# Performance work log

Hardware: AMD Instinct MI355X
Metric: run time of the kernel (lower is better)

## Reference

```python
import jax, jax.numpy as jnp
import numpy as np

# Config
D = 2048; H = 16; HD = 128; L = 2; V = 32000
BS = 16              # KV-cache block (page) size
B = 16               # decode batch (one query token per sequence)
MAXCTX = 1024; NBLK = MAXCTX // BS; NUMBLOCKS = B * NBLK
FF = 4 * D           # swiglu ff_proj width; ff_out input = FF // 2
ALIBI_BIAS_MAX = 8.0
EPS = 1e-5
NEG = -1e30


def alibi_slopes(n_heads, bias_max):
    # n_heads=16 is a power of two -> simple form
    m = jnp.arange(1, n_heads + 1, dtype=jnp.float32) * (bias_max / n_heads)
    return 1.0 / jnp.power(2.0, m)


def ln(x):
    # non-parametric LayerNorm (OLMo default: no affine, no bias)
    mu = jnp.mean(x, axis=-1, keepdims=True)
    var = jnp.var(x, axis=-1, keepdims=True)
    return (x - mu) * jax.lax.rsqrt(var + EPS)


def setup_inputs() -> dict:
    key = jax.random.key(0)
    ks = jax.random.split(key, 12)
    # context_lens includes the current (query) token; >= 1
    context_lens = jax.random.randint(ks[0], (B,), 1, MAXCTX + 1).astype(jnp.int32)
    positions = context_lens - 1                      # 0-indexed position of query token
    block_tables = jnp.arange(B * NBLK, dtype=jnp.int32).reshape(B, NBLK)
    slot_mapping = (block_tables[jnp.arange(B), positions // BS] * BS
                    + positions % BS).astype(jnp.int32)
    input_ids = jax.random.randint(ks[1], (B,), 0, V).astype(jnp.int32)
    s = 0.02
    return {
        "input_ids": input_ids,
        "positions": positions,
        "block_tables": block_tables,
        "context_lens": context_lens,
        "slot_mapping": slot_mapping,
        "wte": jax.random.normal(ks[2], (V, D), jnp.float32) * s,
        "Wq": jax.random.normal(ks[3], (L, D, D), jnp.float32) * s,
        "Wkv": jax.random.normal(ks[4], (L, D, 2 * HD), jnp.float32) * s,
        "Wo": jax.random.normal(ks[5], (L, D, D), jnp.float32) * s,
        "Wff1": jax.random.normal(ks[6], (L, D, FF), jnp.float32) * s,
        "Wff2": jax.random.normal(ks[7], (L, FF // 2, D), jnp.float32) * s,
        "k_caches": jax.random.normal(ks[8], (L, NUMBLOCKS, BS, H, HD), jnp.float32) * 0.1,
        "v_caches": jax.random.normal(ks[9], (L, NUMBLOCKS, BS, H, HD), jnp.float32) * 0.1,
    }


def reference(input_ids, positions, block_tables, context_lens, slot_mapping,
              wte, Wq, Wkv, Wo, Wff1, Wff2, k_caches, v_caches):
    scale = HD ** -0.5
    slopes = alibi_slopes(H, ALIBI_BIAS_MAX)          # [H]
    blk = slot_mapping // BS
    off = slot_mapping % BS
    pos = jnp.arange(MAXCTX)                          # [S]
    valid = pos[None, :] < context_lens[:, None]      # [B,S]
    # ALiBi decode bias: slope * (pos - (ctx_len-1)) for pos < ctx_len
    bias = slopes[None, :, None] * (pos[None, None, :]
            - (context_lens - 1)[:, None, None]).astype(jnp.float32)  # [B,H,S]

    x = wte[input_ids]                                # [B,D]
    for l in range(L):
        t = ln(x)
        q = (t @ Wq[l]).reshape(B, H, HD)
        kv = t @ Wkv[l]
        k_new, v_new = kv[:, :HD], kv[:, HD:]
        # MQA: single kv head repeated across H heads (as k.repeat(1, n_heads))
        k_rep = jnp.broadcast_to(k_new[:, None, :], (B, H, HD))
        v_rep = jnp.broadcast_to(v_new[:, None, :], (B, H, HD))
        # write current token's k/v into paged cache
        kc = k_caches[l].at[blk, off].set(k_rep)      # [NUMBLOCKS,BS,H,HD]
        vc = v_caches[l].at[blk, off].set(v_rep)
        # gather pages per sequence -> [B, MAXCTX, H, HD]
        keys = kc[block_tables].reshape(B, MAXCTX, H, HD)
        vals = vc[block_tables].reshape(B, MAXCTX, H, HD)
        scores = jnp.einsum('bhd,bshd->bhs', q, keys) * scale + bias
        scores = jnp.where(valid[:, None, :], scores, NEG)
        attn = jax.nn.softmax(scores, axis=-1)
        out = jnp.einsum('bhs,bshd->bhd', attn, vals).reshape(B, D)
        x = x + out @ Wo[l]
        h = ln(x) @ Wff1[l]                           # [B,FF]
        a, g = jnp.split(h, 2, axis=-1)               # swiglu: silu(gate) * x
        x = x + (jax.nn.silu(g) * a) @ Wff2[l]
    x = ln(x)
    return x @ wte.T                                  # tied-embedding logits [B,V]
```

## Files before the change

### kernel.cpp

```cpp
#include <hip/hip_runtime.h>
#include <hip/hip_bf16.h>
#include <math.h>

#define D 2048
#define H_ 16
#define HD 128
#define L_ 2
#define V_ 32000
#define BS_ 16
#define B_ 16
#define MAXCTX 1024
#define NBLK 64
#define FF 8192
#define SPLITS 8
#define CHUNK 128

__global__ void ln_kernel(const float* __restrict__ X,
                          const int* __restrict__ ids,
                          const float* __restrict__ wte,
                          float* __restrict__ Xout,
                          float* __restrict__ T,
                          float* __restrict__ Z, int zfloats) {
  if (blockIdx.x >= B_) {
    int nb = gridDim.x - B_;
    int idx = (blockIdx.x - B_) * 256 + threadIdx.x;
    int n4 = zfloats >> 2;
    float4* z4 = (float4*)Z;
    for (int i = idx; i < n4; i += nb * 256) z4[i] = make_float4(0.f, 0.f, 0.f, 0.f);
    return;
  }
  __shared__ float red[8];
  int b = blockIdx.x, tid = threadIdx.x;
  int wid = tid >> 6, lane = tid & 63;
  const float4* src = (const float4*)(ids ? (wte + (size_t)ids[b] * D) : (X + (size_t)b * D));
  float4 v0 = src[tid], v1 = src[tid + 256];
  if (ids) {
    float4* xo = (float4*)(Xout + (size_t)b * D);
    xo[tid] = v0; xo[tid + 256] = v1;
  }
  float s = v0.x + v0.y + v0.z + v0.w + v1.x + v1.y + v1.z + v1.w;
#pragma unroll
  for (int m = 32; m; m >>= 1) s += __shfl_xor(s, m);
  if (lane == 0) red[wid] = s;
  __syncthreads();
  float mu = (red[0] + red[1] + red[2] + red[3]) * (1.f / D);
  float d0 = v0.x - mu, d1 = v0.y - mu, d2 = v0.z - mu, d3 = v0.w - mu;
  float d4 = v1.x - mu, d5 = v1.y - mu, d6 = v1.z - mu, d7 = v1.w - mu;
  float vs = d0*d0 + d1*d1 + d2*d2 + d3*d3 + d4*d4 + d5*d5 + d6*d6 + d7*d7;
#pragma unroll
  for (int m = 32; m; m >>= 1) vs += __shfl_xor(vs, m);
  if (lane == 0) red[4 + wid] = vs;
  __syncthreads();
  float var = (red[4] + red[5] + red[6] + red[7]) * (1.f / D);
  float r = 1.f / sqrtf(var + 1e-5f);
  float4* t4 = (float4*)(T + (size_t)b * D);
  t4[tid]       = make_float4(d0 * r, d1 * r, d2 * r, d3 * r);
  t4[tid + 256] = make_float4(d4 * r, d5 * r, d6 * r, d7 * r);
}

#define GEMM_CORE_STORE(TL, WP, NSTRIDE, OPTR, J)                                  \
  {                                                                                \
    float acc[16];                                                                 \
    _Pragma("unroll") for (int b = 0; b < 16; b++) acc[b] = 0.f;                   \
    const float* wp_ = (WP);                                                       \
    _Pragma("unroll 4") for (int k = 0; k < 64; k++) {                             \
      float w = wp_[(size_t)k * (NSTRIDE)];                                        \
      const float4* tr = (const float4*)(&TL[k][0]);                               \
      float4 t0 = tr[0], t1 = tr[1], t2 = tr[2], t3 = tr[3];                       \
      acc[0]  += t0.x * w; acc[1]  += t0.y * w; acc[2]  += t0.z * w; acc[3]  += t0.w * w; \
      acc[4]  += t1.x * w; acc[5]  += t1.y * w; acc[6]  += t1.z * w; acc[7]  += t1.w * w; \
      acc[8]  += t2.x * w; acc[9]  += t2.y * w; acc[10] += t2.z * w; acc[11] += t2.w * w; \
      acc[12] += t3.x * w; acc[13] += t3.y * w; acc[14] += t3.z * w; acc[15] += t3.w * w; \
    }                                                                              \
    _Pragma("unroll") for (int b = 0; b < 16; b++)                                 \
      atomicAdd(&(OPTR)[(size_t)b * (NSTRIDE) + (J)], acc[b]);                     \
  }

__global__ void gemm_acc_kernel(const float* __restrict__ T,
                                const float* __restrict__ W,
                                float* __restrict__ O,
                                int K, int N) {
  __shared__ __align__(16) float tl[64][20];
  int tid = threadIdx.x;
  int j = blockIdx.x * 256 + tid;
  int k0 = blockIdx.y * 64;
#pragma unroll
  for (int r = 0; r < 4; r++) {
    int ii = tid + r * 256;
    int b = ii >> 6, k = ii & 63;
    tl[k][b] = T[(size_t)b * K + k0 + k];
  }
  __syncthreads();
  GEMM_CORE_STORE(tl, W + (size_t)k0 * N + j, N, O, j)
}

__global__ void qkv_gemm_kernel(const float* __restrict__ T,
                                const float* __restrict__ Wq,
                                const float* __restrict__ Wkv,
                                float* __restrict__ Qo,
                                float* __restrict__ KVo) {
  __shared__ __align__(16) float tl[64][20];
  int tid = threadIdx.x;
  int k0 = blockIdx.y * 64;
#pragma unroll
  for (int r = 0; r < 4; r++) {
    int ii = tid + r * 256;
    int b = ii >> 6, k = ii & 63;
    tl[k][b] = T[(size_t)b * D + k0 + k];
  }
  __syncthreads();
  if (blockIdx.x < 8) {
    int j = blockIdx.x * 256 + tid;
    GEMM_CORE_STORE(tl, Wq + (size_t)k0 * D + j, D, Qo, j)
  } else {
    int j = tid;
    GEMM_CORE_STORE(tl, Wkv + (size_t)k0 * 256 + j, 256, KVo, j)
  }
}

__global__ void attn_split_kernel(const float* __restrict__ Q,
                                  const float* __restrict__ KVn,
                                  const float* __restrict__ KC,
                                  const float* __restrict__ VC,
                                  const int* __restrict__ BT,
                                  const int* __restrict__ CL,
                                  float* __restrict__ Pout,
                                  float* __restrict__ Pms) {
  int bh = blockIdx.x, sp = blockIdx.y;
  int b = bh >> 4, h = bh & 15;
  int ctx = CL[b];
  int s0 = sp * CHUNK;
  if (s0 >= ctx) return;
  int s1 = min(s0 + CHUNK, ctx);
  int n = s1 - s0;
  int last = ctx - 1;
  int tid = threadIdx.x, wid = tid >> 6, lane = tid & 63;
  int half = lane >> 5, l32 = lane & 31;
  __shared__ float sc[CHUNK];
  __shared__ int btl[8];
  __shared__ float4 red[4][64];
  __shared__ float stat[8];
  if (tid < 8) btl[tid] = BT[b * NBLK + sp * 8 + tid];
  __syncthreads();
  float slope = exp2f(-0.5f * (float)(h + 1));
  const float scl = 0.08838834764831845f;
  float4 q4 = ((const float4*)(Q + (size_t)b * D + h * HD))[l32];

  for (int base = s0 + wid * 2; base < s1; base += 8) {
    int ps = base + half;
    if (ps < s1) {
      const float* kp = (ps == last) ? KVn + b * 256
                      : KC + ((size_t)btl[(ps - s0) >> 4] * BS_ + (ps & 15)) * (H_ * HD) + h * HD;
      float4 k4 = ((const float4*)kp)[l32];
      float p = q4.x * k4.x + q4.y * k4.y + q4.z * k4.z + q4.w * k4.w;
#pragma unroll
      for (int m = 16; m; m >>= 1) p += __shfl_xor(p, m);
      if (l32 == 0) sc[ps - s0] = p * scl + slope * (float)(ps - last);
    }
  }
  __syncthreads();

  float mx = -1e30f;
  for (int i = tid; i < n; i += 256) mx = fmaxf(mx, sc[i]);
#pragma unroll
  for (int m = 32; m; m >>= 1) mx = fmaxf(mx, __shfl_xor(mx, m));
  if (lane == 0) stat[wid] = mx;
  __syncthreads();
  mx = fmaxf(fmaxf(stat[0], stat[1]), fmaxf(stat[2], stat[3]));
  float sum = 0.f;
  for (int i = tid; i < n; i += 256) { float e = expf(sc[i] - mx); sc[i] = e; sum += e; }
#pragma unroll
  for (int m = 32; m; m >>= 1) sum += __shfl_xor(sum, m);
  if (lane == 0) stat[4 + wid] = sum;
  __syncthreads();

  float4 a4 = make_float4(0.f, 0.f, 0.f, 0.f);
  for (int base = s0 + wid * 2; base < s1; base += 8) {
    int ps = base + half;
    if (ps < s1) {
      const float* vp = (ps == last) ? KVn + b * 256 + HD
                      : VC + ((size_t)btl[(ps - s0) >> 4] * BS_ + (ps & 15)) * (H_ * HD) + h * HD;
      float4 v4 = ((const float4*)vp)[l32];
      float p = sc[ps - s0];
      a4.x += p * v4.x; a4.y += p * v4.y; a4.z += p * v4.z; a4.w += p * v4.w;
    }
  }
  red[wid][lane] = a4;
  __syncthreads();
  if (tid < 32) {
    float4 o = make_float4(0.f, 0.f, 0.f, 0.f);
#pragma unroll
    for (int w = 0; w < 4; w++) {
      float4 r0 = red[w][tid], r1 = red[w][tid + 32];
      o.x += r0.x + r1.x; o.y += r0.y + r1.y;
      o.z += r0.z + r1.z; o.w += r0.w + r1.w;
    }
    ((float4*)(Pout + ((size_t)(bh * SPLITS + sp) << 7)))[tid] = o;
  }
  if (tid == 0) {
    Pms[(bh * SPLITS + sp) * 2 + 0] = mx;
    Pms[(bh * SPLITS + sp) * 2 + 1] = stat[4] + stat[5] + stat[6] + stat[7];
  }
}

__global__ void wo_gemm_kernel(const float* __restrict__ Pout,
                               const float* __restrict__ Pms,
                               const int* __restrict__ CL,
                               const float* __restrict__ W,
                               float* __restrict__ X) {
  __shared__ __align__(16) float tl[64][20];
  __shared__ float wgt[16][8];
  __shared__ int nspl[16];
  int tid = threadIdx.x;
  int j = blockIdx.x * 256 + tid;
  int k0 = blockIdx.y * 64;
  int h = k0 >> 7, dd0 = k0 & 127;
  if (tid < 16) {
    int ctx = CL[tid];
    int nsp = (ctx + CHUNK - 1) >> 7;
    nspl[tid] = nsp;
    int bh = tid * 16 + h;
    float M = -1e30f;
#pragma unroll
    for (int i = 0; i < 8; i++) {
      float mi = (i < nsp) ? Pms[(bh * SPLITS + i) * 2] : -1e30f;
      M = fmaxf(M, mi);
    }
    float tot = 0.f, e[8];
#pragma unroll
    for (int i = 0; i < 8; i++) {
      float mi = (i < nsp) ? Pms[(bh * SPLITS + i) * 2] : -1e30f;
      float si = (i < nsp) ? Pms[(bh * SPLITS + i) * 2 + 1] : 0.f;
      e[i] = (i < nsp) ? expf(mi - M) : 0.f;
      tot += e[i] * si;
    }
    float inv = 1.f / tot;
#pragma unroll
    for (int i = 0; i < 8; i++) wgt[tid][i] = e[i] * inv;
  }
  __syncthreads();
#pragma unroll
  for (int r = 0; r < 4; r++) {
    int ii = tid + r * 256;
    int b = ii >> 6, k = ii & 63;
    int bh = b * 16 + h;
    int ns = nspl[b];
    float v = 0.f;
    for (int i = 0; i < ns; i++)
      v += wgt[b][i] * Pout[((size_t)(bh * SPLITS + i) << 7) + dd0 + k];
    tl[k][b] = v;
  }
  __syncthreads();
  GEMM_CORE_STORE(tl, W + (size_t)k0 * D + j, D, X, j)
}

__global__ void ff2_gemm_kernel(const float* __restrict__ Hb,
                                const float* __restrict__ W,
                                float* __restrict__ X) {
  __shared__ __align__(16) float tl[64][20];
  int tid = threadIdx.x;
  int j = blockIdx.x * 256 + tid;
  int k0 = blockIdx.y * 64;
#pragma unroll
  for (int r = 0; r < 4; r++) {
    int ii = tid + r * 256;
    int b = ii >> 6, k = ii & 63;
    float a = Hb[(size_t)b * FF + k0 + k];
    float g = Hb[(size_t)b * FF + 4096 + k0 + k];
    tl[k][b] = a * (g / (1.f + expf(-g)));
  }
  __syncthreads();
  GEMM_CORE_STORE(tl, W + (size_t)k0 * D + j, D, X, j)
}

__global__ __launch_bounds__(256, 2)
void logits_kernel(const float* __restrict__ T,
                   const float* __restrict__ wte,
                   float* __restrict__ O) {
  int tid = threadIdx.x;
  int wid = tid >> 6, lane = tid & 63;
  int vbase = blockIdx.x * 16 + wid * 4;
  const float4* T4 = (const float4*)T;
  const float4* W4 = (const float4*)(wte + (size_t)vbase * D);
  float acc[64];
#pragma unroll
  for (int j = 0; j < 64; j++) acc[j] = 0.f;

#pragma unroll 2
  for (int it = 0; it < 8; it++) {
    int idx = it * 64 + lane;
    float4 w0 = W4[idx];
    float4 w1 = W4[512 + idx];
    float4 w2 = W4[1024 + idx];
    float4 w3 = W4[1536 + idx];
#pragma unroll
    for (int b = 0; b < 16; b++) {
      float4 t4 = T4[b * 512 + idx];
      acc[b * 4 + 0] += t4.x * w0.x + t4.y * w0.y + t4.z * w0.z + t4.w * w0.w;
      acc[b * 4 + 1] += t4.x * w1.x + t4.y * w1.y + t4.z * w1.z + t4.w * w1.w;
      acc[b * 4 + 2] += t4.x * w2.x + t4.y * w2.y + t4.z * w2.z + t4.w * w2.w;
      acc[b * 4 + 3] += t4.x * w3.x + t4.y * w3.y + t4.z * w3.z + t4.w * w3.w;
    }
  }

#pragma unroll
  for (int st = 0; st < 6; st++) {
    const int m = 1 << st;
    const int nn = 64 >> (st + 1);
    const bool hi = (lane & m) != 0;
#pragma unroll
    for (int i = 0; i < nn; i++) {
      float a = acc[2 * i], b = acc[2 * i + 1];
      float send = hi ? a : b;
      float keep = hi ? b : a;
      acc[i] = keep + __shfl_xor(send, m);
    }
  }
  O[(size_t)(lane >> 2) * V_ + vbase + (lane & 3)] = acc[0];
}

extern "C" void kernel_launch(void* const* d_in, const int* in_sizes, int n_in,
                              void* d_out, int out_size, void* d_ws, size_t ws_size,
                              hipStream_t stream) {
  const int* ids   = (const int*)d_in[0];
  const int* bt    = (const int*)d_in[2];
  const int* cl    = (const int*)d_in[3];
  const float* wte = (const float*)d_in[5];
  const float* Wq  = (const float*)d_in[6];
  const float* Wkv = (const float*)d_in[7];
  const float* Wo  = (const float*)d_in[8];
  const float* Wff1= (const float*)d_in[9];
  const float* Wff2= (const float*)d_in[10];
  const float* KC  = (const float*)d_in[11];
  const float* VC  = (const float*)d_in[12];
  float* out = (float*)d_out;
  float* ws  = (float*)d_ws;

  float* x    = ws;
  float* t    = ws + 32768;
  float* q    = ws + 65536;
  float* kv   = ws + 98304;
  float* hb   = ws + 135168;
  float* pout = ws + 331776;
  float* pms  = ws + 593920;

  for (int l = 0; l < L_; l++) {
    ln_kernel<<<16 + 64, 256, 0, stream>>>(x, l == 0 ? ids : nullptr, wte, x, t, q, 32768 + 4096);
    qkv_gemm_kernel<<<dim3(9, 32), 256, 0, stream>>>(t, Wq + (size_t)l * 4194304,
                                                     Wkv + (size_t)l * 524288, q, kv);
    attn_split_kernel<<<dim3(256, SPLITS), 256, 0, stream>>>(q, kv,
                                         KC + (size_t)l * 33554432,
                                         VC + (size_t)l * 33554432,
                                         bt, cl, pout, pms);
    wo_gemm_kernel<<<dim3(8, 32), 256, 0, stream>>>(pout, pms, cl, Wo + (size_t)l * 4194304, x);
    ln_kernel<<<16 + 128, 256, 0, stream>>>(x, nullptr, wte, x, t, hb, 131072);
    gemm_acc_kernel<<<dim3(32, 32), 256, 0, stream>>>(t, Wff1 + (size_t)l * 16777216, hb, 2048, 8192);
    ff2_gemm_kernel<<<dim3(8, 64), 256, 0, stream>>>(hb, Wff2 + (size_t)l * 8388608, x);
  }
  ln_kernel<<<16, 256, 0, stream>>>(x, nullptr, wte, x, t, (float*)nullptr, 0);
  logits_kernel<<<2000, 256, 0, stream>>>(t, wte, out);
}
```

Measured before the change: 331.8 us.

## Split K across wavefronts and reduce partials in LDS before atomics

Each GEMM block now covers 64 output columns and a 256-deep K slice, with the four wavefronts each taking a 64-row K sub-slice. Their partial sums are combined in shared memory before one atomicAdd per output. This cuts global atomic traffic by four and gives each block a larger K chunk of activations to reuse. In exchange each wavefront reads only 64 consecutive floats per weight row, which narrows coalescing, and an extra LDS buffer plus a barrier are added.

```diff
diff --git a/kernel.cpp b/kernel.cpp
--- a/kernel.cpp
+++ b/kernel.cpp
@@ -58,40 +58,48 @@
   t4[tid + 256] = make_float4(d4 * r, d5 * r, d6 * r, d7 * r);
 }
 
-#define GEMM_CORE_STORE(TL, WP, NSTRIDE, OPTR, J)                                  \
+#define GEMM256_TAIL(TL, COMB, WP, NSTRIDE, OPTR, JBASE, C, P, TID)                \
   {                                                                                \
     float acc[16];                                                                 \
     _Pragma("unroll") for (int b = 0; b < 16; b++) acc[b] = 0.f;                   \
     const float* wp_ = (WP);                                                       \
     _Pragma("unroll 4") for (int k = 0; k < 64; k++) {                             \
       float w = wp_[(size_t)k * (NSTRIDE)];                                        \
-      const float4* tr = (const float4*)(&TL[k][0]);                               \
+      const float4* tr = (const float4*)(&TL[(P) * 64 + k][0]);                    \
       float4 t0 = tr[0], t1 = tr[1], t2 = tr[2], t3 = tr[3];                       \
       acc[0]  += t0.x * w; acc[1]  += t0.y * w; acc[2]  += t0.z * w; acc[3]  += t0.w * w; \
       acc[4]  += t1.x * w; acc[5]  += t1.y * w; acc[6]  += t1.z * w; acc[7]  += t1.w * w; \
       acc[8]  += t2.x * w; acc[9]  += t2.y * w; acc[10] += t2.z * w; acc[11] += t2.w * w; \
       acc[12] += t3.x * w; acc[13] += t3.y * w; acc[14] += t3.z * w; acc[15] += t3.w * w; \
     }                                                                              \
-    _Pragma("unroll") for (int b = 0; b < 16; b++)                                 \
-      atomicAdd(&(OPTR)[(size_t)b * (NSTRIDE) + (J)], acc[b]);                     \
-  }
-
-__global__ void gemm_acc_kernel(const float* __restrict__ T,
-                                const float* __restrict__ W,
-                                float* __restrict__ O,
-                                int K, int N) {
-  __shared__ __align__(16) float tl[64][20];
-  int tid = threadIdx.x;
-  int j = blockIdx.x * 256 + tid;
-  int k0 = blockIdx.y * 64;
-#pragma unroll
-  for (int r = 0; r < 4; r++) {
+    _Pragma("unroll") for (int b = 0; b < 16; b++) COMB[P][(C) * 17 + b] = acc[b]; \
+    __syncthreads();                                                               \
+    _Pragma("unroll") for (int r = 0; r < 4; r++) {                                \
+      int o = r * 256 + (TID);                                                     \
+      int bb = o >> 6, cc = o & 63;                                                \
+      float v = COMB[0][cc*17+bb] + COMB[1][cc*17+bb] + COMB[2][cc*17+bb] + COMB[3][cc*17+bb]; \
+      atomicAdd(&(OPTR)[(size_t)bb * (NSTRIDE) + (JBASE) + cc], v);                \
+    }                                                                              \
+  }
+
+__global__ void gemm256_kernel(const float* __restrict__ T,
+                               const float* __restrict__ W,
+                               float* __restrict__ O,
+                               int K, int N) {
+  __shared__ __align__(16) float tl[256][20];
+  __shared__ float comb[4][64 * 17];
+  int tid = threadIdx.x;
+  int c = tid & 63, p = tid >> 6;
+  int jbase = blockIdx.x * 64;
+  int k0 = blockIdx.y * 256;
+#pragma unroll
+  for (int r = 0; r < 16; r++) {
     int ii = tid + r * 256;
-    int b = ii >> 6, k = ii & 63;
+    int b = ii >> 8, k = ii & 255;
     tl[k][b] = T[(size_t)b * K + k0 + k];
   }
   __syncthreads();
-  GEMM_CORE_STORE(tl, W + (size_t)k0 * N + j, N, O, j)
+  GEMM256_TAIL(tl, comb, W + (size_t)(k0 + p * 64) * N + jbase + c, N, O, jbase, c, p, tid)
 }
 
 __global__ void qkv_gemm_kernel(const float* __restrict__ T,
@@ -99,22 +107,24 @@
                                 const float* __restrict__ Wkv,
                                 float* __restrict__ Qo,
                                 float* __restrict__ KVo) {
-  __shared__ __align__(16) float tl[64][20];
-  int tid = threadIdx.x;
-  int k0 = blockIdx.y * 64;
-#pragma unroll
-  for (int r = 0; r < 4; r++) {
+  __shared__ __align__(16) float tl[256][20];
+  __shared__ float comb[4][64 * 17];
+  int tid = threadIdx.x;
+  int c = tid & 63, p = tid >> 6;
+  int k0 = blockIdx.y * 256;
+#pragma unroll
+  for (int r = 0; r < 16; r++) {
     int ii = tid + r * 256;
-    int b = ii >> 6, k = ii & 63;
+    int b = ii >> 8, k = ii & 255;
     tl[k][b] = T[(size_t)b * D + k0 + k];
   }
   __syncthreads();
-  if (blockIdx.x < 8) {
-    int j = blockIdx.x * 256 + tid;
-    GEMM_CORE_STORE(tl, Wq + (size_t)k0 * D + j, D, Qo, j)
+  if (blockIdx.x < 32) {
+    int jbase = blockIdx.x * 64;
+    GEMM256_TAIL(tl, comb, Wq + (size_t)(k0 + p * 64) * D + jbase + c, D, Qo, jbase, c, p, tid)
   } else {
-    int j = tid;
-    GEMM_CORE_STORE(tl, Wkv + (size_t)k0 * 256 + j, 256, KVo, j)
+    int jbase = (blockIdx.x - 32) * 64;
+    GEMM256_TAIL(tl, comb, Wkv + (size_t)(k0 + p * 64) * 256 + jbase + c, 256, KVo, jbase, c, p, tid)
   }
 }
 
@@ -208,18 +218,22 @@
                                const int* __restrict__ CL,
                                const float* __restrict__ W,
                                float* __restrict__ X) {
-  __shared__ __align__(16) float tl[64][20];
-  __shared__ float wgt[16][8];
+  __shared__ __align__(16) float tl[256][20];
+  __shared__ float comb[4][64 * 17];
+  __shared__ float wgt[16][2][8];
   __shared__ int nspl[16];
   int tid = threadIdx.x;
-  int j = blockIdx.x * 256 + tid;
-  int k0 = blockIdx.y * 64;
-  int h = k0 >> 7, dd0 = k0 & 127;
-  if (tid < 16) {
-    int ctx = CL[tid];
+  int c = tid & 63, p = tid >> 6;
+  int jbase = blockIdx.x * 64;
+  int k0 = blockIdx.y * 256;
+  int h0 = k0 >> 7;
+  if (tid < 32) {
+    int b = tid & 15, hh = tid >> 4;
+    int h = h0 + hh;
+    int ctx = CL[b];
     int nsp = (ctx + CHUNK - 1) >> 7;
-    nspl[tid] = nsp;
-    int bh = tid * 16 + h;
+    if (hh == 0) nspl[b] = nsp;
+    int bh = b * 16 + h;
     float M = -1e30f;
 #pragma unroll
     for (int i = 0; i < 8; i++) {
@@ -236,41 +250,44 @@
     }
     float inv = 1.f / tot;
 #pragma unroll
-    for (int i = 0; i < 8; i++) wgt[tid][i] = e[i] * inv;
-  }
-  __syncthreads();
-#pragma unroll
-  for (int r = 0; r < 4; r++) {
+    for (int i = 0; i < 8; i++) wgt[b][hh][i] = e[i] * inv;
+  }
+  __syncthreads();
+#pragma unroll
+  for (int r = 0; r < 16; r++) {
     int ii = tid + r * 256;
-    int b = ii >> 6, k = ii & 63;
-    int bh = b * 16 + h;
+    int b = ii >> 8, k = ii & 255;
+    int hh = k >> 7, dd = k & 127;
+    int bh = b * 16 + h0 + hh;
     int ns = nspl[b];
     float v = 0.f;
     for (int i = 0; i < ns; i++)
-      v += wgt[b][i] * Pout[((size_t)(bh * SPLITS + i) << 7) + dd0 + k];
+      v += wgt[b][hh][i] * Pout[((size_t)(bh * SPLITS + i) << 7) + dd];
     tl[k][b] = v;
   }
   __syncthreads();
-  GEMM_CORE_STORE(tl, W + (size_t)k0 * D + j, D, X, j)
+  GEMM256_TAIL(tl, comb, W + (size_t)(k0 + p * 64) * D + jbase + c, D, X, jbase, c, p, tid)
 }
 
 __global__ void ff2_gemm_kernel(const float* __restrict__ Hb,
                                 const float* __restrict__ W,
                                 float* __restrict__ X) {
-  __shared__ __align__(16) float tl[64][20];
-  int tid = threadIdx.x;
-  int j = blockIdx.x * 256 + tid;
-  int k0 = blockIdx.y * 64;
-#pragma unroll
-  for (int r = 0; r < 4; r++) {
+  __shared__ __align__(16) float tl[256][20];
+  __shared__ float comb[4][64 * 17];
+  int tid = threadIdx.x;
+  int c = tid & 63, p = tid >> 6;
+  int jbase = blockIdx.x * 64;
+  int k0 = blockIdx.y * 256;
+#pragma unroll
+  for (int r = 0; r < 16; r++) {
     int ii = tid + r * 256;
-    int b = ii >> 6, k = ii & 63;
+    int b = ii >> 8, k = ii & 255;
     float a = Hb[(size_t)b * FF + k0 + k];
     float g = Hb[(size_t)b * FF + 4096 + k0 + k];
     tl[k][b] = a * (g / (1.f + expf(-g)));
   }
   __syncthreads();
-  GEMM_CORE_STORE(tl, W + (size_t)k0 * D + j, D, X, j)
+  GEMM256_TAIL(tl, comb, W + (size_t)(k0 + p * 64) * D + jbase + c, D, X, jbase, c, p, tid)
 }
 
 __global__ __launch_bounds__(256, 2)
@@ -346,16 +363,16 @@
 
   for (int l = 0; l < L_; l++) {
     ln_kernel<<<16 + 64, 256, 0, stream>>>(x, l == 0 ? ids : nullptr, wte, x, t, q, 32768 + 4096);
-    qkv_gemm_kernel<<<dim3(9, 32), 256, 0, stream>>>(t, Wq + (size_t)l * 4194304,
+    qkv_gemm_kernel<<<dim3(36, 8), 256, 0, stream>>>(t, Wq + (size_t)l * 4194304,
                                                      Wkv + (size_t)l * 524288, q, kv);
     attn_split_kernel<<<dim3(256, SPLITS), 256, 0, stream>>>(q, kv,
                                          KC + (size_t)l * 33554432,
                                          VC + (size_t)l * 33554432,
                                          bt, cl, pout, pms);
-    wo_gemm_kernel<<<dim3(8, 32), 256, 0, stream>>>(pout, pms, cl, Wo + (size_t)l * 4194304, x);
+    wo_gemm_kernel<<<dim3(32, 8), 256, 0, stream>>>(pout, pms, cl, Wo + (size_t)l * 4194304, x);
     ln_kernel<<<16 + 128, 256, 0, stream>>>(x, nullptr, wte, x, t, hb, 131072);
-    gemm_acc_kernel<<<dim3(32, 32), 256, 0, stream>>>(t, Wff1 + (size_t)l * 16777216, hb, 2048, 8192);
-    ff2_gemm_kernel<<<dim3(8, 64), 256, 0, stream>>>(hb, Wff2 + (size_t)l * 8388608, x);
+    gemm256_kernel<<<dim3(128, 8), 256, 0, stream>>>(t, Wff1 + (size_t)l * 16777216, hb, 2048, 8192);
+    ff2_gemm_kernel<<<dim3(32, 16), 256, 0, stream>>>(hb, Wff2 + (size_t)l * 8388608, x);
   }
   ln_kernel<<<16, 256, 0, stream>>>(x, nullptr, wte, x, t, (float*)nullptr, 0);
   logits_kernel<<<2000, 256, 0, stream>>>(t, wte, out);
```

Result: no change. 325.8 us (median of 2 runs) (-1.8%).
